# Optimization experiments

Measured on AMD Instinct MI355X. Metric: run time of the kernel, lower is better.

Reference implementation:

```python
import jax, jax.numpy as jnp
import numpy as np

B, V, M, H, T = 512, 256, 128, 512, 16  # batch, vocab, memory_size, hidden_dim, timing_dim
ALPHA = 0.95


def setup_inputs() -> dict:
    key = jax.random.key(0)
    ks = jax.random.split(key, 8)
    return {
        "x": jax.random.uniform(ks[0], (B, V), dtype=jnp.float32),
        "memory": jax.random.normal(ks[1], (B, M, V), dtype=jnp.float32),
        "memory_timings": jax.random.randint(ks[2], (B, M), 0, 1000, dtype=jnp.int64) if jax.config.jax_enable_x64 else jax.random.randint(ks[2], (B, M), 0, 1000).astype(jnp.int32),
        "memory_surprise": jax.random.uniform(ks[3], (B, M), dtype=jnp.float32),
        "last_prediction": jax.random.uniform(ks[4], (B, V), dtype=jnp.float32),
        "W1": jax.random.normal(ks[5], (V * M + M * T, H), dtype=jnp.float32) * 0.01,
        "b1": jnp.zeros((H,), dtype=jnp.float32),
        "W2": jax.random.normal(ks[6], (H, V), dtype=jnp.float32) * 0.01,
        "b2": jnp.zeros((V,), dtype=jnp.float32),
    }


def reference(x, memory, memory_timings, memory_surprise, last_prediction, W1, b1, W2, b2):
    b = x.shape[0]
    ar = jnp.arange(b)
    # compute_surprise
    surprise = -jnp.sum(x * jnp.log(last_prediction + 1e-6), axis=1)  # [B]
    # update_memory_timings
    timings = memory_timings + 1
    msurp = memory_surprise * ALPHA
    # update_memory: argmin-scatter into memory/timings/surprise
    idx = jnp.argmin(msurp, axis=1)  # [B]
    memory = memory.at[ar, idx].set(x)
    timings = timings.at[ar, idx].set(0)
    msurp = msurp.at[ar, idx].set(surprise)
    # compute_prediction: sort by timing, gather-reorder memory
    order = jnp.argsort(timings, axis=1)  # stable ascending, [B, M]
    sorted_t = jnp.take_along_axis(timings, order, axis=1)  # [B, M]
    sorted_mem = jnp.take_along_axis(memory, order[:, :, None], axis=1)  # [B, M, V]
    # binary encoding of timings: (t // 2**k) % 2 for k in [0, T)
    bits = ((sorted_t[:, :, None] >> jnp.arange(T)) & 1).astype(jnp.float32)  # [B, M, T]
    pred_in = jnp.concatenate([sorted_mem.reshape(b, -1), bits.reshape(b, -1)], axis=1)
    h = jax.nn.relu(pred_in @ W1 + b1)
    return h @ W2 + b2
```

## Files before the change

kernel.cpp:

```cpp
#include <hip/hip_runtime.h>

typedef unsigned int uint;
typedef unsigned short ushort;
typedef __attribute__((ext_vector_type(8))) short short8;
typedef __attribute__((ext_vector_type(4))) float f32x4;

#define B_   512
#define V_   256
#define M_   128
#define H_   512
#define T_   16
#define KTOT 34816

__device__ __forceinline__ ushort f2bf(float f) {
  uint u = __builtin_bit_cast(uint, f);
  u += 0x7fffu + ((u >> 16) & 1u);
  return (ushort)(u >> 16);
}
__device__ __forceinline__ float bf2f(ushort s) {
  return __builtin_bit_cast(float, ((uint)s) << 16);
}

__device__ __forceinline__ int swz_k(int k, int row) {
  return (k & ~31) | (((((k >> 3) & 3) ^ ((row >> 1) & 3)) << 3)) | (k & 7);
}

__global__ __launch_bounds__(256) void prep_kernel(
    const float* __restrict__ x, const float* __restrict__ mem,
    const int* __restrict__ timings, const float* __restrict__ msurp,
    const float* __restrict__ b1,
    ushort* __restrict__ A, float* __restrict__ h_pre)
{
  const int b = blockIdx.x, tid = threadIdx.x;
  __shared__ int s_t[M_];
  __shared__ int s_row[M_];
  __shared__ int s_st[M_];
  __shared__ int s_idx;

  if (tid < 64) {
    float v0 = msurp[b * M_ + tid];
    float v1 = msurp[b * M_ + tid + 64];
    float v; int i;
    if (v1 < v0) { v = v1; i = tid + 64; } else { v = v0; i = tid; }
    #pragma unroll
    for (int off = 32; off > 0; off >>= 1) {
      float ov = __shfl_down(v, off);
      int   oi = __shfl_down(i, off);
      if (ov < v || (ov == v && oi < i)) { v = ov; i = oi; }
    }
    if (tid == 0) s_idx = i;
  }
  __syncthreads();
  const int idx = s_idx;

  if (tid < M_) {
    int t = timings[b * M_ + tid] + 1;
    if (tid == idx) t = 0;
    s_t[tid] = t;
  }
  h_pre[(size_t)b * H_ + tid]       = b1[tid];
  h_pre[(size_t)b * H_ + 256 + tid] = b1[256 + tid];
  __syncthreads();

  if (tid < M_) {
    const int t = s_t[tid];
    int r = 0;
    for (int j = 0; j < M_; ++j) {
      int tj = s_t[j];
      r += (tj < t || (tj == t && j < tid)) ? 1 : 0;
    }
    s_row[r] = tid;
    s_st[r]  = t;
  }
  __syncthreads();

  if (tid < M_) {
    const int t = s_st[tid];
    uint p[8];
    #pragma unroll
    for (int h = 0; h < 8; ++h) {
      uint lo = ((t >> (2 * h)) & 1) ? 0x3F80u : 0u;
      uint hi = ((t >> (2 * h + 1)) & 1) ? 0x3F80u : 0u;
      p[h] = lo | (hi << 16);
    }
    const int k0 = V_ * M_ + tid * T_;
    uint4 w0; w0.x = p[0]; w0.y = p[1]; w0.z = p[2]; w0.w = p[3];
    uint4 w1; w1.x = p[4]; w1.y = p[5]; w1.z = p[6]; w1.w = p[7];
    *(uint4*)(A + (size_t)b * KTOT + swz_k(k0, b))     = w0;
    *(uint4*)(A + (size_t)b * KTOT + swz_k(k0 + 8, b)) = w1;
  }

  const int lane = tid & 63, sub = tid >> 6;
  for (int it = 0; it < 32; ++it) {
    const int slot = it * 4 + sub;
    const int rowm = s_row[slot];
    const float* src = (rowm == idx) ? (x + (size_t)b * V_)
                                     : (mem + ((size_t)b * M_ + rowm) * V_);
    f32x4 v = *(const f32x4*)(src + lane * 4);
    uint2 o;
    o.x = (uint)f2bf(v[0]) | ((uint)f2bf(v[1]) << 16);
    o.y = (uint)f2bf(v[2]) | ((uint)f2bf(v[3]) << 16);
    const int k = slot * V_ + lane * 4;
    *(uint2*)(A + (size_t)b * KTOT + swz_k(k, b)) = o;
  }
}

#define BM 512
#define BN 128
#define SPLITK 64
#define KCH 544
#define NCHU 17

#define GLD16(g, l) __builtin_amdgcn_global_load_lds( \
  (const __attribute__((address_space(1))) void*)(g), \
  (__attribute__((address_space(3))) void*)(l), 16, 0, 0)

template<bool USE_ATOMIC>
__global__ __launch_bounds__(512, 2) void gemm1_kernel(
    const ushort* __restrict__ A, const float* __restrict__ W1,
    void* __restrict__ dstv)
{
  __shared__ __align__(16) ushort As[3][BM * 32];
  __shared__ __align__(16) ushort Bs[2][BN * 32];

  const int bid  = blockIdx.x;
  const int sk   = (bid & 7) | ((bid >> 5) << 3);
  const int tile = (bid >> 3) & 3;
  const int n0   = tile * BN;
  const int tid  = threadIdx.x, wave = tid >> 6, lane = tid & 63;
  const long kb0 = (long)sk * KCH;

  f32x4 acc[4][8];
  #pragma unroll
  for (int i = 0; i < 4; ++i)
    #pragma unroll
    for (int j = 0; j < 8; ++j) acc[i][j] = (f32x4)0.f;

  const int ar  = wave * 64 + (lane >> 2);
  const int akk = (lane & 3) * 8;
  auto stageA = [&](int buf, int chunk) {
    const long kb = kb0 + (long)chunk * 32;
    #pragma unroll
    for (int q = 0; q < 4; ++q)
      GLD16(A + ((size_t)(ar + q * 16)) * KTOT + kb + akk,
            &As[buf][(wave * 64 + q * 16) * 32]);
  };

  const int ncol = tid & 127;
  const int koct = tid >> 7;
  const float* w1p = W1 + (size_t)(kb0 + koct * 8) * H_ + n0 + ncol;
  const int b_woff = ncol * 32 + ((koct ^ ((ncol >> 1) & 3)) * 8);

  auto loadB = [&](float* r, int c) {
    const float* p = w1p + (size_t)c * 32 * H_;
    #pragma unroll
    for (int i = 0; i < 8; ++i) r[i] = p[(size_t)i * H_];
  };
  auto writeB = [&](const float* r, ushort* base) {
    uint4 o;
    o.x = (uint)f2bf(r[0]) | ((uint)f2bf(r[1]) << 16);
    o.y = (uint)f2bf(r[2]) | ((uint)f2bf(r[3]) << 16);
    o.z = (uint)f2bf(r[4]) | ((uint)f2bf(r[5]) << 16);
    o.w = (uint)f2bf(r[6]) | ((uint)f2bf(r[7]) << 16);
    *(uint4*)(base + b_woff) = o;
  };

  const int xo     = (((lane >> 4) ^ ((lane >> 1) & 3)) * 8);
  const int a_roff = (wave * 64 + (lane & 15)) * 32;
  const int b_roff = (lane & 15) * 32;

  float brE[8], brO[8];

#define GITER(c, BRL, BRW, ISSUE, WRITE, VMC) do {                            \
    asm volatile("s_waitcnt vmcnt(" VMC ") lgkmcnt(0)" ::: "memory");         \
    __builtin_amdgcn_s_barrier();                                             \
    __builtin_amdgcn_sched_barrier(0);                                        \
    if (ISSUE) { stageA(((c) + 2) % 3, (c) + 2); loadB(BRL, (c) + 2); }       \
    const ushort* as_ = &As[(c) % 3][a_roff + xo];                            \
    const ushort* bs_ = &Bs[(c) & 1][b_roff + xo];                            \
    short8 af[4], bf[4];                                                      \
    _Pragma("unroll") for (int i = 0; i < 4; ++i)                             \
      af[i] = *(const short8*)(as_ + i * 16 * 32);                            \
    _Pragma("unroll") for (int j = 0; j < 4; ++j)                             \
      bf[j] = *(const short8*)(bs_ + j * 16 * 32);                            \
    _Pragma("unroll") for (int i = 0; i < 4; ++i)                             \
      _Pragma("unroll") for (int j = 0; j < 4; ++j)                           \
        acc[i][j] = __builtin_amdgcn_mfma_f32_16x16x32_bf16(af[i], bf[j],     \
                                                            acc[i][j], 0,0,0);\
    _Pragma("unroll") for (int j = 0; j < 4; ++j)                             \
      bf[j] = *(const short8*)(bs_ + (j + 4) * 16 * 32);                      \
    _Pragma("unroll") for (int i = 0; i < 4; ++i)                             \
      _Pragma("unroll") for (int j = 0; j < 4; ++j)                           \
        acc[i][j + 4] = __builtin_amdgcn_mfma_f32_16x16x32_bf16(af[i], bf[j], \
                                                            acc[i][j + 4],    \
                                                            0, 0, 0);         \
    if (WRITE) writeB(BRW, &Bs[((c) + 1) & 1][0]);                            \
  } while (0)

  stageA(0, 0);
  loadB(brE, 0);
  stageA(1, 1);
  loadB(brO, 1);
  writeB(brE, &Bs[0][0]);

  #pragma unroll 1
  for (int cc = 0; cc < 14; cc += 2) {
    GITER(cc,     brE, brO, true, true, "12");
    GITER(cc + 1, brO, brE, true, true, "12");
  }
  GITER(14, brE, brO, true,  true,  "12");
  GITER(15, brO, brE, false, true,  "12");
  GITER(16, brE, brO, false, false, "0");
#undef GITER

  const int row0 = wave * 64 + (lane >> 4) * 4;
  const int col0 = n0 + (lane & 15);
  if constexpr (USE_ATOMIC) {
    float* dst = (float*)dstv;
    #pragma unroll
    for (int i = 0; i < 4; ++i)
      #pragma unroll
      for (int j = 0; j < 8; ++j)
        #pragma unroll
        for (int r = 0; r < 4; ++r)
          atomicAdd(&dst[(size_t)(row0 + i * 16 + r) * H_ + col0 + j * 16], acc[i][j][r]);
  } else {
    ushort* P = (ushort*)dstv + (size_t)sk * (B_ * H_);
    #pragma unroll
    for (int i = 0; i < 4; ++i)
      #pragma unroll
      for (int j = 0; j < 8; ++j)
        #pragma unroll
        for (int r = 0; r < 4; ++r)
          P[(size_t)(row0 + i * 16 + r) * H_ + col0 + j * 16] = f2bf(acc[i][j][r]);
  }
}

template<bool FROM_PARTIALS>
__global__ __launch_bounds__(256) void gemm2_kernel(
    const void* __restrict__ Pin, const float* __restrict__ b1,
    const float* __restrict__ W2, const float* __restrict__ b2,
    float* __restrict__ out)
{
  const int bb = blockIdx.x * 2;
  const int v  = threadIdx.x;
  __shared__ float hs[2][H_];

  {
    const int id  = v * 4;
    const int row = id >> 9, col = id & 511;
    f32x4 s;
    if constexpr (FROM_PARTIALS) {
      const ushort* P = (const ushort*)Pin;
      s = *(const f32x4*)(b1 + col);
      #pragma unroll 4
      for (int sk = 0; sk < SPLITK; ++sk) {
        uint2 u = *(const uint2*)(P + (size_t)sk * (B_ * H_) + (size_t)(bb + row) * H_ + col);
        s[0] += bf2f((ushort)(u.x & 0xffff));
        s[1] += bf2f((ushort)(u.x >> 16));
        s[2] += bf2f((ushort)(u.y & 0xffff));
        s[3] += bf2f((ushort)(u.y >> 16));
      }
    } else {
      s = *(const f32x4*)((const float*)Pin + (size_t)(bb + row) * H_ + col);
    }
    f32x4 r;
    #pragma unroll
    for (int t = 0; t < 4; ++t) r[t] = fmaxf(s[t], 0.f);
    *(f32x4*)&hs[row][col] = r;
  }
  __syncthreads();

  float a0 = 0.f, a1 = 0.f;
  for (int j4 = 0; j4 < H_ / 4; ++j4) {
    f32x4 h0 = *(const f32x4*)&hs[0][j4 * 4];
    f32x4 h1 = *(const f32x4*)&hs[1][j4 * 4];
    #pragma unroll
    for (int t = 0; t < 4; ++t) {
      float w = W2[(size_t)(j4 * 4 + t) * V_ + v];
      a0 += h0[t] * w; a1 += h1[t] * w;
    }
  }
  const float bias = b2[v];
  out[(size_t)(bb + 0) * V_ + v] = a0 + bias;
  out[(size_t)(bb + 1) * V_ + v] = a1 + bias;
}

extern "C" void kernel_launch(void* const* d_in, const int* in_sizes, int n_in,
                              void* d_out, int out_size, void* d_ws, size_t ws_size,
                              hipStream_t stream) {
  const float* x   = (const float*)d_in[0];
  const float* mem = (const float*)d_in[1];
  const int*   tim = (const int*)d_in[2];
  const float* msu = (const float*)d_in[3];
  const float* W1  = (const float*)d_in[5];
  const float* b1  = (const float*)d_in[6];
  const float* W2  = (const float*)d_in[7];
  const float* b2  = (const float*)d_in[8];
  float* out = (float*)d_out;

  char* ws = (char*)d_ws;
  const size_t abytes = (size_t)B_ * KTOT * 2;
  const size_t pbytes = (size_t)SPLITK * B_ * H_ * 2;
  const size_t hbytes = (size_t)B_ * H_ * 4;
  const bool partials = ws_size >= abytes + pbytes + hbytes;

  ushort* A_ws  = (ushort*)ws;
  void*   P     = (void*)(ws + abytes);
  float*  h_pre = partials ? (float*)(ws + abytes + pbytes)
                           : (float*)(ws + abytes);

  prep_kernel<<<B_, 256, 0, stream>>>(x, mem, tim, msu, b1, A_ws, h_pre);
  if (partials) {
    gemm1_kernel<false><<<4 * SPLITK, 512, 0, stream>>>(A_ws, W1, P);
    gemm2_kernel<true><<<B_ / 2, 256, 0, stream>>>(P, b1, W2, b2, out);
  } else {
    gemm1_kernel<true><<<4 * SPLITK, 512, 0, stream>>>(A_ws, W1, h_pre);
    gemm2_kernel<false><<<B_ / 2, 256, 0, stream>>>(h_pre, b1, W2, b2, out);
  }
}
```

Measured before the change: 75.19 us.

## Double K-chunk size to 64 in split-K GEMM1 main loop with tail chunk

Restructures the split-K GEMM1 pipeline to stage 64-wide K chunks instead of 32. This halves the number of barrier/wait iterations: 8 full chunks plus a 32-wide tail replace 17 small chunks. A and B LDS buffers become double-buffered at twice the width, and B prefetch registers grow to 16 floats per buffer. The goal is to cut synchronization overhead per MFMA, at the cost of a shallower A pipeline (2 buffers instead of 3), more LDS and more register pressure, which could hurt the two-blocks-per-CU occupancy.

```diff
diff --git a/kernel.cpp b/kernel.cpp
--- a/kernel.cpp
+++ b/kernel.cpp
@@ -109,7 +109,7 @@
 #define BN 128
 #define SPLITK 64
 #define KCH 544
-#define NCHU 17
+#define NFULL 8
 
 #define GLD16(g, l) __builtin_amdgcn_global_load_lds( \
   (const __attribute__((address_space(1))) void*)(g), \
@@ -120,8 +120,8 @@
     const ushort* __restrict__ A, const float* __restrict__ W1,
     void* __restrict__ dstv)
 {
-  __shared__ __align__(16) ushort As[3][BM * 32];
-  __shared__ __align__(16) ushort Bs[2][BN * 32];
+  __shared__ __align__(16) ushort As[2][BM * 64];
+  __shared__ __align__(16) ushort Bs[2][BN * 64];
 
   const int bid  = blockIdx.x;
   const int sk   = (bid & 7) | ((bid >> 5) << 3);
@@ -136,82 +136,145 @@
     #pragma unroll
     for (int j = 0; j < 8; ++j) acc[i][j] = (f32x4)0.f;
 
-  const int ar  = wave * 64 + (lane >> 2);
-  const int akk = (lane & 3) * 8;
-  auto stageA = [&](int buf, int chunk) {
-    const long kb = kb0 + (long)chunk * 32;
+  const int ar8  = wave * 64 + (lane >> 3);
+  const int akk8 = (lane & 7) * 8;
+  auto stageA64 = [&](int buf, int c) {
+    const long kb = kb0 + (long)c * 64;
+    #pragma unroll
+    for (int q = 0; q < 8; ++q)
+      GLD16(A + ((size_t)(ar8 + q * 8)) * KTOT + kb + akk8,
+            &As[buf][(wave * 64 + q * 8) * 64]);
+  };
+  const int ar4  = wave * 64 + (lane >> 2);
+  const int akk4 = (lane & 3) * 8;
+  auto stageA32 = [&]() {
+    const long kb = kb0 + 512;
     #pragma unroll
     for (int q = 0; q < 4; ++q)
-      GLD16(A + ((size_t)(ar + q * 16)) * KTOT + kb + akk,
-            &As[buf][(wave * 64 + q * 16) * 32]);
+      GLD16(A + ((size_t)(ar4 + q * 16)) * KTOT + kb + akk4,
+            &As[0][(wave * 64 + q * 16) * 32]);
   };
 
   const int ncol = tid & 127;
   const int koct = tid >> 7;
-  const float* w1p = W1 + (size_t)(kb0 + koct * 8) * H_ + n0 + ncol;
-  const int b_woff = ncol * 32 + ((koct ^ ((ncol >> 1) & 3)) * 8);
-
-  auto loadB = [&](float* r, int c) {
-    const float* p = w1p + (size_t)c * 32 * H_;
-    #pragma unroll
-    for (int i = 0; i < 8; ++i) r[i] = p[(size_t)i * H_];
-  };
-  auto writeB = [&](const float* r, ushort* base) {
+  const int sg   = (ncol >> 1) & 3;
+  const float* w1p  = W1 + (size_t)(kb0 + koct * 16) * H_ + n0 + ncol;
+  const float* w1pt = W1 + (size_t)(kb0 + 512 + koct * 8) * H_ + n0 + ncol;
+  const int g64 = (koct >> 1), c064 = (koct & 1) * 2;
+  const int bw0 = ncol * 64 + g64 * 32 + ((c064 ^ sg) * 8);
+  const int bw1 = ncol * 64 + g64 * 32 + (((c064 + 1) ^ sg) * 8);
+  const int bwt = ncol * 32 + ((koct ^ sg) * 8);
+
+  auto loadB64 = [&](float* r, int c) {
+    const float* p = w1p + (size_t)c * 64 * H_;
+    #pragma unroll
+    for (int i = 0; i < 16; ++i) r[i] = p[(size_t)i * H_];
+  };
+  auto writeB64 = [&](const float* r, ushort* base) {
+    uint4 o0, o1;
+    o0.x = (uint)f2bf(r[0])  | ((uint)f2bf(r[1])  << 16);
+    o0.y = (uint)f2bf(r[2])  | ((uint)f2bf(r[3])  << 16);
+    o0.z = (uint)f2bf(r[4])  | ((uint)f2bf(r[5])  << 16);
+    o0.w = (uint)f2bf(r[6])  | ((uint)f2bf(r[7])  << 16);
+    o1.x = (uint)f2bf(r[8])  | ((uint)f2bf(r[9])  << 16);
+    o1.y = (uint)f2bf(r[10]) | ((uint)f2bf(r[11]) << 16);
+    o1.z = (uint)f2bf(r[12]) | ((uint)f2bf(r[13]) << 16);
+    o1.w = (uint)f2bf(r[14]) | ((uint)f2bf(r[15]) << 16);
+    *(uint4*)(base + bw0) = o0;
+    *(uint4*)(base + bw1) = o1;
+  };
+  auto loadB32 = [&](float* r) {
+    #pragma unroll
+    for (int i = 0; i < 8; ++i) r[i] = w1pt[(size_t)i * H_];
+  };
+  auto writeB32 = [&](const float* r, ushort* base) {
     uint4 o;
     o.x = (uint)f2bf(r[0]) | ((uint)f2bf(r[1]) << 16);
     o.y = (uint)f2bf(r[2]) | ((uint)f2bf(r[3]) << 16);
     o.z = (uint)f2bf(r[4]) | ((uint)f2bf(r[5]) << 16);
     o.w = (uint)f2bf(r[6]) | ((uint)f2bf(r[7]) << 16);
-    *(uint4*)(base + b_woff) = o;
-  };
-
-  const int xo     = (((lane >> 4) ^ ((lane >> 1) & 3)) * 8);
-  const int a_roff = (wave * 64 + (lane & 15)) * 32;
-  const int b_roff = (lane & 15) * 32;
-
-  float brE[8], brO[8];
-
-#define GITER(c, BRL, BRW, ISSUE, WRITE, VMC) do {                            \
+    *(uint4*)(base + bwt) = o;
+  };
+
+  const int xo    = (((lane >> 4) ^ ((lane >> 1) & 3)) * 8);
+  const int a_ro  = (wave * 64 + (lane & 15)) * 64;
+  const int b_ro  = (lane & 15) * 64;
+
+  float brE[16], brO[16], brT[8];
+
+#define FITER(C, BRL, BRW, ISSA, ISSB, ISSBT, ISSAT, W64, W32, VMC) do {      \
     asm volatile("s_waitcnt vmcnt(" VMC ") lgkmcnt(0)" ::: "memory");         \
     __builtin_amdgcn_s_barrier();                                             \
     __builtin_amdgcn_sched_barrier(0);                                        \
-    if (ISSUE) { stageA(((c) + 2) % 3, (c) + 2); loadB(BRL, (c) + 2); }       \
-    const ushort* as_ = &As[(c) % 3][a_roff + xo];                            \
-    const ushort* bs_ = &Bs[(c) & 1][b_roff + xo];                            \
-    short8 af[4], bf[4];                                                      \
-    _Pragma("unroll") for (int i = 0; i < 4; ++i)                             \
-      af[i] = *(const short8*)(as_ + i * 16 * 32);                            \
-    _Pragma("unroll") for (int j = 0; j < 4; ++j)                             \
-      bf[j] = *(const short8*)(bs_ + j * 16 * 32);                            \
-    _Pragma("unroll") for (int i = 0; i < 4; ++i)                             \
+    if (ISSA)  stageA64(((C) + 1) & 1, (C) + 1);                              \
+    if (ISSB)  loadB64(BRL, (C) + 2);                                         \
+    if (ISSBT) loadB32(brT);                                                  \
+    if (ISSAT) stageA32();                                                    \
+    _Pragma("unroll") for (int h = 0; h < 2; ++h) {                           \
+      const ushort* as_ = &As[(C) & 1][a_ro + h * 32 + xo];                   \
+      const ushort* bs_ = &Bs[(C) & 1][b_ro + h * 32 + xo];                   \
+      short8 af[4], bf[4];                                                    \
+      _Pragma("unroll") for (int i = 0; i < 4; ++i)                           \
+        af[i] = *(const short8*)(as_ + i * 16 * 64);                          \
       _Pragma("unroll") for (int j = 0; j < 4; ++j)                           \
-        acc[i][j] = __builtin_amdgcn_mfma_f32_16x16x32_bf16(af[i], bf[j],     \
-                                                            acc[i][j], 0,0,0);\
-    _Pragma("unroll") for (int j = 0; j < 4; ++j)                             \
-      bf[j] = *(const short8*)(bs_ + (j + 4) * 16 * 32);                      \
-    _Pragma("unroll") for (int i = 0; i < 4; ++i)                             \
+        bf[j] = *(const short8*)(bs_ + j * 16 * 64);                          \
+      _Pragma("unroll") for (int i = 0; i < 4; ++i)                           \
+        _Pragma("unroll") for (int j = 0; j < 4; ++j)                         \
+          acc[i][j] = __builtin_amdgcn_mfma_f32_16x16x32_bf16(af[i], bf[j],   \
+                                                          acc[i][j], 0,0,0);  \
       _Pragma("unroll") for (int j = 0; j < 4; ++j)                           \
-        acc[i][j + 4] = __builtin_amdgcn_mfma_f32_16x16x32_bf16(af[i], bf[j], \
-                                                            acc[i][j + 4],    \
-                                                            0, 0, 0);         \
-    if (WRITE) writeB(BRW, &Bs[((c) + 1) & 1][0]);                            \
+        bf[j] = *(const short8*)(bs_ + (j + 4) * 16 * 64);                    \
+      _Pragma("unroll") for (int i = 0; i < 4; ++i)                           \
+        _Pragma("unroll") for (int j = 0; j < 4; ++j)                         \
+          acc[i][j + 4] = __builtin_amdgcn_mfma_f32_16x16x32_bf16(af[i],      \
+                                               bf[j], acc[i][j + 4], 0,0,0);  \
+    }                                                                         \
+    if (W64) writeB64(BRW, &Bs[((C) + 1) & 1][0]);                            \
+    if (W32) writeB32(brT, &Bs[0][0]);                                        \
   } while (0)
 
-  stageA(0, 0);
-  loadB(brE, 0);
-  stageA(1, 1);
-  loadB(brO, 1);
-  writeB(brE, &Bs[0][0]);
-
-  #pragma unroll 1
-  for (int cc = 0; cc < 14; cc += 2) {
-    GITER(cc,     brE, brO, true, true, "12");
-    GITER(cc + 1, brO, brE, true, true, "12");
-  }
-  GITER(14, brE, brO, true,  true,  "12");
-  GITER(15, brO, brE, false, true,  "12");
-  GITER(16, brE, brO, false, false, "0");
-#undef GITER
+  loadB64(brE, 0);
+  stageA64(0, 0);
+  loadB64(brO, 1);
+  writeB64(brE, &Bs[0][0]);
+
+  FITER(0, brE, brO, true,  true,  false, false, true,  false, "16");
+  FITER(1, brO, brE, true,  true,  false, false, true,  false, "16");
+  FITER(2, brE, brO, true,  true,  false, false, true,  false, "16");
+  FITER(3, brO, brE, true,  true,  false, false, true,  false, "16");
+  FITER(4, brE, brO, true,  true,  false, false, true,  false, "16");
+  FITER(5, brO, brE, true,  true,  false, false, true,  false, "16");
+  FITER(6, brE, brO, true,  false, true,  false, true,  false, "16");
+  FITER(7, brO, brE, false, false, false, true,  false, true,  "8");
+#undef FITER
+
+  {
+    asm volatile("s_waitcnt vmcnt(0) lgkmcnt(0)" ::: "memory");
+    __builtin_amdgcn_s_barrier();
+    __builtin_amdgcn_sched_barrier(0);
+    const ushort* as_ = &As[0][(wave * 64 + (lane & 15)) * 32 + xo];
+    const ushort* bs_ = &Bs[0][(lane & 15) * 32 + xo];
+    short8 af[4], bf[4];
+    #pragma unroll
+    for (int i = 0; i < 4; ++i)
+      af[i] = *(const short8*)(as_ + i * 16 * 32);
+    #pragma unroll
+    for (int j = 0; j < 4; ++j)
+      bf[j] = *(const short8*)(bs_ + j * 16 * 32);
+    #pragma unroll
+    for (int i = 0; i < 4; ++i)
+      #pragma unroll
+      for (int j = 0; j < 4; ++j)
+        acc[i][j] = __builtin_amdgcn_mfma_f32_16x16x32_bf16(af[i], bf[j], acc[i][j], 0, 0, 0);
+    #pragma unroll
+    for (int j = 0; j < 4; ++j)
+      bf[j] = *(const short8*)(bs_ + (j + 4) * 16 * 32);
+    #pragma unroll
+    for (int i = 0; i < 4; ++i)
+      #pragma unroll
+      for (int j = 0; j < 4; ++j)
+        acc[i][j + 4] = __builtin_amdgcn_mfma_f32_16x16x32_bf16(af[i], bf[j], acc[i][j + 4], 0, 0, 0);
+  }
 
   const int row0 = wave * 64 + (lane >> 4) * 4;
   const int col0 = n0 + (lane & 15);
```

Measured after the change: 92.06 us. 22.4% more time.
